# Kernel tuning notes

Hardware: AMD Instinct MI355X
Metric: run time of the kernel (lower is better)

## Reference

```python
import jax, jax.numpy as jnp
import numpy as np

N_NODES = 50000
N_EDGES = 800000
D_IN, D_HID, D_OUT = 128, 128, 64


def setup_inputs() -> dict:
    key = jax.random.key(0)
    ks = jax.random.split(key, 10)
    return {
        "x": jax.random.normal(ks[0], (N_NODES, D_IN), dtype=jnp.float32),
        "edge_row": jax.random.randint(ks[1], (N_EDGES,), 0, N_NODES, dtype=jnp.int32),
        "edge_col": jax.random.randint(ks[2], (N_EDGES,), 0, N_NODES, dtype=jnp.int32),
        "edge_val": jax.random.uniform(ks[3], (N_EDGES,), dtype=jnp.float32),
        "W1": jax.random.normal(ks[4], (D_IN, D_HID), dtype=jnp.float32) * (1.0 / np.sqrt(D_HID)),
        "b1": jax.random.normal(ks[5], (D_HID,), dtype=jnp.float32) * (1.0 / np.sqrt(D_HID)),
        "W2": jax.random.normal(ks[6], (D_HID, D_HID), dtype=jnp.float32) * (1.0 / np.sqrt(D_HID)),
        "b2": jax.random.normal(ks[7], (D_HID,), dtype=jnp.float32) * (1.0 / np.sqrt(D_HID)),
        "W3": jax.random.normal(ks[8], (D_HID, D_OUT), dtype=jnp.float32) * (1.0 / np.sqrt(D_OUT)),
        "b3": jax.random.normal(ks[9], (D_OUT,), dtype=jnp.float32) * (1.0 / np.sqrt(D_OUT)),
    }


def _gcn_layer(x, edge_row, edge_col, edge_val, W, b):
    # support = x @ W          : dense GEMM [N, d_out]
    support = x @ W
    # spmm(adj, support)[i] = sum_e with row[e]==i: val[e] * support[col[e]]
    gathered = support[edge_col] * edge_val[:, None]  # [E, d_out]
    agg = jax.ops.segment_sum(gathered, edge_row, num_segments=x.shape[0])
    return agg + b


def reference(x, edge_row, edge_col, edge_val, W1, b1, W2, b2, W3, b3):
    # Layer 1 + ReLU (dropout is identity in eval)
    h = jax.nn.relu(_gcn_layer(x, edge_row, edge_col, edge_val, W1, b1))
    # Layer 2 + ReLU
    h = jax.nn.relu(_gcn_layer(h, edge_row, edge_col, edge_val, W2, b2))
    # Layer 3 (no activation)
    return _gcn_layer(h, edge_row, edge_col, edge_val, W3, b3)
```

## Files before the change

### kernel.cpp

```cpp
#include <hip/hip_runtime.h>

#define N_NODES 50000
#define N_EDGES 800000
#define GEMM1_BLOCKS 704
#define FUSED_BLOCKS 512
#define FILL_BLOCKS ((N_EDGES + 255) / 256)
#define SCAN_BLOCKS ((N_NODES + 255) / 256)

#define HB 64
#define EPB (N_EDGES / HB)
#define HGROUPS (EPB / 4)
#define HWORDS (N_NODES / 4)

static_assert(N_NODES < 65536, "col must fit in 16 bits for packed CSR");
static_assert(N_EDGES % (4 * HB) == 0, "chunking must be exact");

typedef __attribute__((ext_vector_type(4))) float f32x4;
typedef __attribute__((ext_vector_type(8))) short bf16x8;

__device__ inline unsigned short f32_to_bf16(float f) {
    unsigned int u = __builtin_bit_cast(unsigned int, f);
    u += 0x7FFF + ((u >> 16) & 1);
    return (unsigned short)(u >> 16);
}
__device__ inline float bf16_to_f32(unsigned short h) {
    unsigned int u = ((unsigned int)h) << 16;
    return __builtin_bit_cast(float, u);
}

template <int NOUT>
__device__ __forceinline__ void mfma_phase(const unsigned short* Xs,
                                           const unsigned short* Ws,
                                           unsigned short* __restrict__ Yb,
                                           int block_row, int N) {
    constexpr int KP = 128 + 8;
    constexpr int NT = NOUT / 16;
    const int tid = threadIdx.x;
    const int wave = tid >> 6;
    const int lane = tid & 63;
    const int m = lane & 15;
    const int quad = lane >> 4;
    const int rowbase = wave * 16;

    f32x4 acc[NT];
#pragma unroll
    for (int t = 0; t < NT; ++t) acc[t] = (f32x4){0.f, 0.f, 0.f, 0.f};

#pragma unroll
    for (int kt = 0; kt < 4; ++kt) {
        bf16x8 a = *reinterpret_cast<const bf16x8*>(
            Xs + (rowbase + m) * KP + kt * 32 + quad * 8);
#pragma unroll
        for (int t = 0; t < NT; ++t) {
            bf16x8 b = *reinterpret_cast<const bf16x8*>(
                Ws + (t * 16 + m) * KP + kt * 32 + quad * 8);
            acc[t] = __builtin_amdgcn_mfma_f32_16x16x32_bf16(a, b, acc[t], 0, 0, 0);
        }
    }

#pragma unroll
    for (int t = 0; t < NT; ++t) {
#pragma unroll
        for (int r = 0; r < 4; ++r) {
            int grow = block_row + rowbase + quad * 4 + r;
            if (grow < N)
                Yb[(size_t)grow * NOUT + t * 16 + m] = f32_to_bf16(acc[t][r]);
        }
    }
}

__global__ __launch_bounds__(256) void mega1(
    const float* __restrict__ x, const float* __restrict__ W1,
    unsigned short* __restrict__ Yb, int N, int ntiles_g,
    const int* __restrict__ erow, unsigned int* __restrict__ rank8,
    unsigned int* __restrict__ bhist) {
    constexpr int KP = 128 + 8;
    __shared__ __align__(16) unsigned char smem[52224];
    const int tid = threadIdx.x;

    if (blockIdx.x < HB) {
        const int b = blockIdx.x;
        unsigned int* h = reinterpret_cast<unsigned int*>(smem);
        int4* h4 = reinterpret_cast<int4*>(h);
        for (int i = tid; i < HWORDS / 4; i += 256) {
            int4 z = {0, 0, 0, 0};
            h4[i] = z;
        }
        __syncthreads();
        const int4* eg = reinterpret_cast<const int4*>(erow) + (size_t)b * HGROUPS;
        unsigned int* rg = rank8 + (size_t)b * HGROUPS;
        for (int g = tid; g < HGROUPS; g += 256) {
            int4 er = eg[g];
            unsigned int rk;
            int sh;
            unsigned int o;
            sh = (er.x & 3) << 3;
            o = atomicAdd(&h[er.x >> 2], 1u << sh);
            rk = (o >> sh) & 0xFFu;
            sh = (er.y & 3) << 3;
            o = atomicAdd(&h[er.y >> 2], 1u << sh);
            rk |= ((o >> sh) & 0xFFu) << 8;
            sh = (er.z & 3) << 3;
            o = atomicAdd(&h[er.z >> 2], 1u << sh);
            rk |= ((o >> sh) & 0xFFu) << 16;
            sh = (er.w & 3) << 3;
            o = atomicAdd(&h[er.w >> 2], 1u << sh);
            rk |= ((o >> sh) & 0xFFu) << 24;
            rg[g] = rk;
        }
        __syncthreads();
        int4* dst = reinterpret_cast<int4*>(bhist + (size_t)b * HWORDS);
        for (int i = tid; i < HWORDS / 4; i += 256) dst[i] = h4[i];
        return;
    }

    const int gb = blockIdx.x - HB;
    unsigned short* Xs = reinterpret_cast<unsigned short*>(smem);
    unsigned short* Ws = reinterpret_cast<unsigned short*>(smem) + 64 * KP;

    for (int idx = tid; idx < 128 * 128; idx += 256) {
        int k = idx >> 7, m = idx & 127;
        Ws[m * KP + k] = f32_to_bf16(W1[idx]);
    }

    for (int tile = gb; tile < ntiles_g; tile += GEMM1_BLOCKS) {
        const int block_row = tile * 64;
        for (int idx = tid; idx < 64 * 16; idx += 256) {
            int r = idx >> 4, ch = idx & 15;
            int gr = block_row + r;
            if (gr >= N) gr = N - 1;
            const float4* xp =
                reinterpret_cast<const float4*>(x + (size_t)gr * 128 + ch * 8);
            float4 a = xp[0], b2 = xp[1];
            uint4 o;
            o.x = (unsigned int)f32_to_bf16(a.x) | ((unsigned int)f32_to_bf16(a.y) << 16);
            o.y = (unsigned int)f32_to_bf16(a.z) | ((unsigned int)f32_to_bf16(a.w) << 16);
            o.z = (unsigned int)f32_to_bf16(b2.x) | ((unsigned int)f32_to_bf16(b2.y) << 16);
            o.w = (unsigned int)f32_to_bf16(b2.z) | ((unsigned int)f32_to_bf16(b2.w) << 16);
            *reinterpret_cast<uint4*>(Xs + r * KP + ch * 8) = o;
        }
        __syncthreads();
        mfma_phase<128>(Xs, Ws, Yb, block_row, N);
        __syncthreads();
    }
}

__global__ void scan1(const unsigned int* __restrict__ bhist,
                      int* __restrict__ pref, int* __restrict__ btot, int n) {
    __shared__ int sums[256];
    const int t = threadIdx.x;
    const int b = blockIdx.x;
    const int node = b * 256 + t;
    const unsigned char* bh8 = reinterpret_cast<const unsigned char*>(bhist);
    int deg = 0;
    if (node < n) {
        for (int c = 0; c < HB; ++c) deg += bh8[(size_t)c * N_NODES + node];
    }
    sums[t] = deg;
    __syncthreads();
    for (int off = 1; off < 256; off <<= 1) {
        int x = (t >= off) ? sums[t - off] : 0;
        __syncthreads();
        sums[t] += x;
        __syncthreads();
    }
    if (node < n) pref[node] = sums[t] - deg;
    if (t == 255) btot[b] = sums[255];
}

__global__ void scan2(const unsigned int* __restrict__ bhist,
                      const int* __restrict__ pref, const int* __restrict__ btot,
                      int* __restrict__ rptr, int* __restrict__ bbase,
                      int n, int nblocks) {
    __shared__ int off_s, tot_s;
    const int t = threadIdx.x;
    const int b = blockIdx.x;
    const int node = b * 256 + t;
    if (t == 0) {
        int off = 0, tot = 0;
        for (int i = 0; i < nblocks; ++i) {
            int v = btot[i];
            if (i < b) off += v;
            tot += v;
        }
        off_s = off;
        tot_s = tot;
    }
    __syncthreads();
    if (node < n) {
        int run = off_s + pref[node];
        rptr[node] = run;
        const unsigned char* bh8 = reinterpret_cast<const unsigned char*>(bhist);
        for (int c = 0; c < HB; ++c) {
            bbase[(size_t)c * N_NODES + node] = run;
            run += bh8[(size_t)c * N_NODES + node];
        }
    }
    if (b == 0 && t == 0) rptr[n] = tot_s;
}

__global__ void fill_csr(const int* __restrict__ erow, const int* __restrict__ ecol,
                         const float* __restrict__ eval, const int* __restrict__ bbase,
                         const unsigned int* __restrict__ rank8,
                         unsigned int* __restrict__ cpack) {
    int e = blockIdx.x * blockDim.x + threadIdx.x;
    if (e >= N_EDGES) return;
    const unsigned char* r8 = reinterpret_cast<const unsigned char*>(rank8);
    int slot = bbase[(size_t)(e / EPB) * N_NODES + erow[e]] + r8[e];
    unsigned int p = (unsigned int)(ecol[e] & 0xFFFF) |
                     ((unsigned int)f32_to_bf16(eval[e]) << 16);
    cpack[slot] = p;
}

template <int NOUT>
__device__ __forceinline__ void mfma_phase512(const unsigned short* Xs,
                                              const unsigned short* Ws,
                                              unsigned short* __restrict__ Yb,
                                              int block_row, int N) {
    constexpr int KP = 128 + 8;
    constexpr int NT = NOUT / 16;
    constexpr int NTH = NT / 2;
    const int tid = threadIdx.x;
    const int wave = tid >> 6;
    const int lane = tid & 63;
    const int m = lane & 15;
    const int quad = lane >> 4;
    const int rowbase = (wave & 3) * 16;
    const int tbase = (wave >> 2) * NTH;

    f32x4 acc[NTH];
#pragma unroll
    for (int t = 0; t < NTH; ++t) acc[t] = (f32x4){0.f, 0.f, 0.f, 0.f};

#pragma unroll
    for (int kt = 0; kt < 4; ++kt) {
        bf16x8 a = *reinterpret_cast<const bf16x8*>(
            Xs + (rowbase + m) * KP + kt * 32 + quad * 8);
#pragma unroll
        for (int t = 0; t < NTH; ++t) {
            bf16x8 b = *reinterpret_cast<const bf16x8*>(
                Ws + ((tbase + t) * 16 + m) * KP + kt * 32 + quad * 8);
            acc[t] = __builtin_amdgcn_mfma_f32_16x16x32_bf16(a, b, acc[t], 0, 0, 0);
        }
    }

#pragma unroll
    for (int t = 0; t < NTH; ++t) {
#pragma unroll
        for (int r = 0; r < 4; ++r) {
            int grow = block_row + rowbase + quad * 4 + r;
            if (grow < N)
                Yb[(size_t)grow * NOUT + (tbase + t) * 16 + m] = f32_to_bf16(acc[t][r]);
        }
    }
}

template <int NOUT>
__global__ __launch_bounds__(512, 4) void gemm_fused_agg(
    const unsigned short* __restrict__ S,
    const int* __restrict__ rptr, const unsigned int* __restrict__ cpack,
    const float* __restrict__ bias,
    const float* __restrict__ W,
    unsigned short* __restrict__ Yb,
    int N, int ntiles) {
    constexpr int KP = 128 + 8;
    __shared__ unsigned short Xs[64 * KP];
    __shared__ unsigned short Ws[NOUT * KP];
    __shared__ unsigned int cp_s[2048];
    const int tid = threadIdx.x;
    const int group = tid >> 4;
    const int f8 = tid & 15;

    for (int idx = tid; idx < 128 * NOUT; idx += 512) {
        int k = idx / NOUT, m = idx % NOUT;
        Ws[m * KP + k] = f32_to_bf16(W[idx]);
    }

    float bv[8];
#pragma unroll
    for (int i = 0; i < 8; ++i) bv[i] = bias[f8 * 8 + i];

    for (int tile = blockIdx.x; tile < ntiles; tile += gridDim.x) {
        const int block_row = tile * 64;
        const int rend = (block_row + 64 < N) ? block_row + 64 : N;
        const int ebeg = rptr[block_row];
        const int ecount = rptr[rend] - ebeg;
        __syncthreads();
        for (int i = tid; i < ecount; i += 512) cp_s[i] = cpack[ebeg + i];
        __syncthreads();
#pragma unroll
        for (int r4 = 0; r4 < 2; ++r4) {
            const int row = r4 * 32 + group;
            const int node = block_row + row;
            float acc[8];
#pragma unroll
            for (int i = 0; i < 8; ++i) acc[i] = bv[i];
            if (node < N) {
                const int beg = rptr[node] - ebeg;
                const int end = rptr[node + 1] - ebeg;
                int j = beg;
                for (; j + 8 <= end; j += 8) {
                    unsigned int p[8];
                    uint4 s[8];
#pragma unroll
                    for (int u = 0; u < 8; ++u) p[u] = cp_s[j + u];
#pragma unroll
                    for (int u = 0; u < 8; ++u)
                        s[u] = *reinterpret_cast<const uint4*>(
                            S + (size_t)(p[u] & 0xFFFF) * 128 + f8 * 8);
#pragma unroll
                    for (int u = 0; u < 8; ++u) {
                        const float v = bf16_to_f32((unsigned short)(p[u] >> 16));
                        const unsigned short* sp =
                            reinterpret_cast<const unsigned short*>(&s[u]);
#pragma unroll
                        for (int i = 0; i < 8; ++i)
                            acc[i] = fmaf(v, bf16_to_f32(sp[i]), acc[i]);
                    }
                }
                if (j + 4 <= end) {
                    unsigned int p[4];
                    uint4 s[4];
#pragma unroll
                    for (int u = 0; u < 4; ++u) p[u] = cp_s[j + u];
#pragma unroll
                    for (int u = 0; u < 4; ++u)
                        s[u] = *reinterpret_cast<const uint4*>(
                            S + (size_t)(p[u] & 0xFFFF) * 128 + f8 * 8);
#pragma unroll
                    for (int u = 0; u < 4; ++u) {
                        const float v = bf16_to_f32((unsigned short)(p[u] >> 16));
                        const unsigned short* sp =
                            reinterpret_cast<const unsigned short*>(&s[u]);
#pragma unroll
                        for (int i = 0; i < 8; ++i)
                            acc[i] = fmaf(v, bf16_to_f32(sp[i]), acc[i]);
                    }
                    j += 4;
                }
                if (j + 2 <= end) {
                    unsigned int p[2];
                    uint4 s[2];
#pragma unroll
                    for (int u = 0; u < 2; ++u) p[u] = cp_s[j + u];
#pragma unroll
                    for (int u = 0; u < 2; ++u)
                        s[u] = *reinterpret_cast<const uint4*>(
                            S + (size_t)(p[u] & 0xFFFF) * 128 + f8 * 8);
#pragma unroll
                    for (int u = 0; u < 2; ++u) {
                        const float v = bf16_to_f32((unsigned short)(p[u] >> 16));
                        const unsigned short* sp =
                            reinterpret_cast<const unsigned short*>(&s[u]);
#pragma unroll
                        for (int i = 0; i < 8; ++i)
                            acc[i] = fmaf(v, bf16_to_f32(sp[i]), acc[i]);
                    }
                    j += 2;
                }
                if (j < end) {
                    unsigned int p = cp_s[j];
                    uint4 s = *reinterpret_cast<const uint4*>(
                        S + (size_t)(p & 0xFFFF) * 128 + f8 * 8);
                    const float v = bf16_to_f32((unsigned short)(p >> 16));
                    const unsigned short* sp =
                        reinterpret_cast<const unsigned short*>(&s);
#pragma unroll
                    for (int i = 0; i < 8; ++i)
                        acc[i] = fmaf(v, bf16_to_f32(sp[i]), acc[i]);
                }
            }
            uint4 o;
            o.x = (unsigned int)f32_to_bf16(fmaxf(acc[0], 0.f)) |
                  ((unsigned int)f32_to_bf16(fmaxf(acc[1], 0.f)) << 16);
            o.y = (unsigned int)f32_to_bf16(fmaxf(acc[2], 0.f)) |
                  ((unsigned int)f32_to_bf16(fmaxf(acc[3], 0.f)) << 16);
            o.z = (unsigned int)f32_to_bf16(fmaxf(acc[4], 0.f)) |
                  ((unsigned int)f32_to_bf16(fmaxf(acc[5], 0.f)) << 16);
            o.w = (unsigned int)f32_to_bf16(fmaxf(acc[6], 0.f)) |
                  ((unsigned int)f32_to_bf16(fmaxf(acc[7], 0.f)) << 16);
            *reinterpret_cast<uint4*>(Xs + row * KP + f8 * 8) = o;
        }
        __syncthreads();
        mfma_phase512<NOUT>(Xs, Ws, Yb, block_row, N);
    }
}

__global__ void aggregate_bf16_64(const unsigned short* __restrict__ S,
                                  const int* __restrict__ rptr,
                                  const unsigned int* __restrict__ cpack,
                                  const float* __restrict__ bias,
                                  float* __restrict__ out, int N) {
    __shared__ unsigned int cp_s[1536];
    const int t = threadIdx.x;
    const int nfirst = blockIdx.x * 32;
    const int node = nfirst + (t >> 3);
    const int f8 = t & 7;
    const int nlast1 = (nfirst + 32 < N) ? nfirst + 32 : N;
    int ebeg = 0, ecount = 0;
    if (nfirst < N) {
        ebeg = rptr[nfirst];
        ecount = rptr[nlast1] - ebeg;
    }
    for (int i = t; i < ecount; i += 256) cp_s[i] = cpack[ebeg + i];
    __syncthreads();
    if (node >= N) return;
    int j = rptr[node] - ebeg;
    const int end = rptr[node + 1] - ebeg;
    float acc[8];
#pragma unroll
    for (int i = 0; i < 8; ++i) acc[i] = bias[f8 * 8 + i];
    for (; j + 8 <= end; j += 8) {
        unsigned int p[8];
        uint4 s[8];
#pragma unroll
        for (int u = 0; u < 8; ++u) p[u] = cp_s[j + u];
#pragma unroll
        for (int u = 0; u < 8; ++u)
            s[u] = *reinterpret_cast<const uint4*>(S + (size_t)(p[u] & 0xFFFF) * 64 + f8 * 8);
#pragma unroll
        for (int u = 0; u < 8; ++u) {
            const float v = bf16_to_f32((unsigned short)(p[u] >> 16));
            const unsigned short* sp = reinterpret_cast<const unsigned short*>(&s[u]);
#pragma unroll
            for (int i = 0; i < 8; ++i) acc[i] = fmaf(v, bf16_to_f32(sp[i]), acc[i]);
        }
    }
    if (j + 4 <= end) {
        unsigned int p[4];
        uint4 s[4];
#pragma unroll
        for (int u = 0; u < 4; ++u) p[u] = cp_s[j + u];
#pragma unroll
        for (int u = 0; u < 4; ++u)
            s[u] = *reinterpret_cast<const uint4*>(S + (size_t)(p[u] & 0xFFFF) * 64 + f8 * 8);
#pragma unroll
        for (int u = 0; u < 4; ++u) {
            const float v = bf16_to_f32((unsigned short)(p[u] >> 16));
            const unsigned short* sp = reinterpret_cast<const unsigned short*>(&s[u]);
#pragma unroll
            for (int i = 0; i < 8; ++i) acc[i] = fmaf(v, bf16_to_f32(sp[i]), acc[i]);
        }
        j += 4;
    }
    if (j + 2 <= end) {
        unsigned int p[2];
        uint4 s[2];
#pragma unroll
        for (int u = 0; u < 2; ++u) p[u] = cp_s[j + u];
#pragma unroll
        for (int u = 0; u < 2; ++u)
            s[u] = *reinterpret_cast<const uint4*>(S + (size_t)(p[u] & 0xFFFF) * 64 + f8 * 8);
#pragma unroll
        for (int u = 0; u < 2; ++u) {
            const float v = bf16_to_f32((unsigned short)(p[u] >> 16));
            const unsigned short* sp = reinterpret_cast<const unsigned short*>(&s[u]);
#pragma unroll
            for (int i = 0; i < 8; ++i) acc[i] = fmaf(v, bf16_to_f32(sp[i]), acc[i]);
        }
        j += 2;
    }
    if (j < end) {
        unsigned int p = cp_s[j];
        uint4 s = *reinterpret_cast<const uint4*>(S + (size_t)(p & 0xFFFF) * 64 + f8 * 8);
        const float v = bf16_to_f32((unsigned short)(p >> 16));
        const unsigned short* sp = reinterpret_cast<const unsigned short*>(&s);
#pragma unroll
        for (int i = 0; i < 8; ++i) acc[i] = fmaf(v, bf16_to_f32(sp[i]), acc[i]);
    }
    float4 o0 = {acc[0], acc[1], acc[2], acc[3]};
    float4 o1 = {acc[4], acc[5], acc[6], acc[7]};
    float* op = out + (size_t)node * 64 + f8 * 8;
    *reinterpret_cast<float4*>(op) = o0;
    *reinterpret_cast<float4*>(op + 4) = o1;
}

extern "C" void kernel_launch(void* const* d_in, const int* in_sizes, int n_in,
                              void* d_out, int out_size, void* d_ws, size_t ws_size,
                              hipStream_t stream) {
    const float* x    = (const float*)d_in[0];
    const int*   erow = (const int*)d_in[1];
    const int*   ecol = (const int*)d_in[2];
    const float* eval = (const float*)d_in[3];
    const float* W1   = (const float*)d_in[4];
    const float* b1   = (const float*)d_in[5];
    const float* W2   = (const float*)d_in[6];
    const float* b2   = (const float*)d_in[7];
    const float* W3   = (const float*)d_in[8];
    const float* b3   = (const float*)d_in[9];
    float* out = (float*)d_out;

    const size_t nf = (size_t)N_NODES * 128;
    unsigned short* SA   = (unsigned short*)d_ws;
    unsigned short* SB   = SA + nf;
    unsigned int*  rank8 = (unsigned int*)(SB + nf);
    unsigned int*  bhist = rank8 + N_EDGES / 4;
    int*   bbase  = (int*)(bhist + (size_t)HB * HWORDS);
    int*   rptr   = bbase + (size_t)HB * N_NODES;
    unsigned int* cpack = (unsigned int*)(rptr + N_NODES + 1);
    int*   pref   = (int*)(cpack + N_EDGES);
    int*   btot   = pref + N_NODES;

    const int blk = 256;
    const int ntiles_g = (N_NODES + 63) / 64;
    const int agg_grid = (int)(((long long)N_NODES * 8 + blk - 1) / blk);

    mega1<<<HB + GEMM1_BLOCKS, blk, 0, stream>>>(
        x, W1, SA, N_NODES, ntiles_g, erow, rank8, bhist);

    scan1<<<SCAN_BLOCKS, blk, 0, stream>>>(bhist, pref, btot, N_NODES);
    scan2<<<SCAN_BLOCKS, blk, 0, stream>>>(bhist, pref, btot, rptr, bbase,
                                           N_NODES, SCAN_BLOCKS);

    fill_csr<<<FILL_BLOCKS, blk, 0, stream>>>(erow, ecol, eval, bbase, rank8, cpack);

    gemm_fused_agg<128><<<FUSED_BLOCKS, 512, 0, stream>>>(
        SA, rptr, cpack, b1, W2, SB, N_NODES, ntiles_g);

    gemm_fused_agg<64><<<FUSED_BLOCKS, 512, 0, stream>>>(
        SB, rptr, cpack, b2, W3, SA, N_NODES, ntiles_g);

    aggregate_bf16_64<<<agg_grid, blk, 0, stream>>>(SA, rptr, cpack, b3, out, N_NODES);
}
```

Measured before the change: 218.8 us.

## Fuse CSR scan and fill into mega1 with grid-wide atomic barriers

Merges the two scan kernels and the CSR fill kernel into the first GEMM/histogram kernel. Histogram blocks use device-scope atomic counters as spin barriers to do the degree scan cooperatively, and then all blocks wait before filling the packed CSR. The per-chunk base offsets are now stored as 8-bit cumulative counts (cum8) instead of 32-bit bbase, and the fill processes four edges per thread with vector loads. This removes three kernel launches and shrinks workspace traffic. In exchange it relies on all 768 blocks being co-resident to avoid deadlock, and the GEMM blocks must idle until the scan finishes.

```diff
diff --git a/kernel.cpp b/kernel.cpp
--- a/kernel.cpp
+++ b/kernel.cpp
@@ -4,13 +4,15 @@
 #define N_EDGES 800000
 #define GEMM1_BLOCKS 704
 #define FUSED_BLOCKS 512
-#define FILL_BLOCKS ((N_EDGES + 255) / 256)
-#define SCAN_BLOCKS ((N_NODES + 255) / 256)
 
 #define HB 64
 #define EPB (N_EDGES / HB)
 #define HGROUPS (EPB / 4)
 #define HWORDS (N_NODES / 4)
+#define NGROUPS (N_EDGES / 4)
+#define TOTB (HB + GEMM1_BLOCKS)
+#define GPB ((NGROUPS + TOTB - 1) / TOTB)
+#define SCAN_NPB 800
 
 static_assert(N_NODES < 65536, "col must fit in 16 bits for packed CSR");
 static_assert(N_EDGES % (4 * HB) == 0, "chunking must be exact");
@@ -72,14 +74,20 @@
 __global__ __launch_bounds__(256) void mega1(
     const float* __restrict__ x, const float* __restrict__ W1,
     unsigned short* __restrict__ Yb, int N, int ntiles_g,
-    const int* __restrict__ erow, unsigned int* __restrict__ rank8,
-    unsigned int* __restrict__ bhist) {
+    const int* __restrict__ erow, const int* __restrict__ ecol,
+    const float* __restrict__ eval,
+    unsigned int* __restrict__ rank8, unsigned int* __restrict__ bhist,
+    unsigned char* __restrict__ cum8, int* __restrict__ rptr,
+    unsigned int* __restrict__ cpack, int* __restrict__ btot,
+    int* __restrict__ c_hist, int* __restrict__ c_s1, int* __restrict__ c_s2) {
     constexpr int KP = 128 + 8;
     __shared__ __align__(16) unsigned char smem[52224];
+    __shared__ int off_s;
     const int tid = threadIdx.x;
-
-    if (blockIdx.x < HB) {
-        const int b = blockIdx.x;
+    const int b = blockIdx.x;
+
+    if (b < HB) {
+        if (b == 0 && tid == 0) { *c_hist = 0; *c_s1 = 0; *c_s2 = 0; }
         unsigned int* h = reinterpret_cast<unsigned int*>(smem);
         int4* h4 = reinterpret_cast<int4*>(h);
         for (int i = tid; i < HWORDS / 4; i += 256) {
@@ -111,105 +119,141 @@
         __syncthreads();
         int4* dst = reinterpret_cast<int4*>(bhist + (size_t)b * HWORDS);
         for (int i = tid; i < HWORDS / 4; i += 256) dst[i] = h4[i];
-        return;
-    }
-
-    const int gb = blockIdx.x - HB;
-    unsigned short* Xs = reinterpret_cast<unsigned short*>(smem);
-    unsigned short* Ws = reinterpret_cast<unsigned short*>(smem) + 64 * KP;
-
-    for (int idx = tid; idx < 128 * 128; idx += 256) {
-        int k = idx >> 7, m = idx & 127;
-        Ws[m * KP + k] = f32_to_bf16(W1[idx]);
-    }
-
-    for (int tile = gb; tile < ntiles_g; tile += GEMM1_BLOCKS) {
-        const int block_row = tile * 64;
-        for (int idx = tid; idx < 64 * 16; idx += 256) {
-            int r = idx >> 4, ch = idx & 15;
-            int gr = block_row + r;
-            if (gr >= N) gr = N - 1;
-            const float4* xp =
-                reinterpret_cast<const float4*>(x + (size_t)gr * 128 + ch * 8);
-            float4 a = xp[0], b2 = xp[1];
-            uint4 o;
-            o.x = (unsigned int)f32_to_bf16(a.x) | ((unsigned int)f32_to_bf16(a.y) << 16);
-            o.y = (unsigned int)f32_to_bf16(a.z) | ((unsigned int)f32_to_bf16(a.w) << 16);
-            o.z = (unsigned int)f32_to_bf16(b2.x) | ((unsigned int)f32_to_bf16(b2.y) << 16);
-            o.w = (unsigned int)f32_to_bf16(b2.z) | ((unsigned int)f32_to_bf16(b2.w) << 16);
-            *reinterpret_cast<uint4*>(Xs + r * KP + ch * 8) = o;
-        }
-        __syncthreads();
-        mfma_phase<128>(Xs, Ws, Yb, block_row, N);
-        __syncthreads();
-    }
-}
-
-__global__ void scan1(const unsigned int* __restrict__ bhist,
-                      int* __restrict__ pref, int* __restrict__ btot, int n) {
-    __shared__ int sums[256];
-    const int t = threadIdx.x;
-    const int b = blockIdx.x;
-    const int node = b * 256 + t;
-    const unsigned char* bh8 = reinterpret_cast<const unsigned char*>(bhist);
-    int deg = 0;
-    if (node < n) {
-        for (int c = 0; c < HB; ++c) deg += bh8[(size_t)c * N_NODES + node];
-    }
-    sums[t] = deg;
+        __threadfence();
+        if (tid == 0) atomicAdd(c_hist, 1);
+
+        int* deg_s = reinterpret_cast<int*>(smem);
+        int* sums = deg_s + SCAN_NPB;
+        const int nbase = b * SCAN_NPB;
+        int nlen = N - nbase;
+        if (nlen > SCAN_NPB) nlen = SCAN_NPB;
+        if (nlen < 0) nlen = 0;
+        if (tid == 0) {
+            while (__hip_atomic_load(c_hist, __ATOMIC_ACQUIRE,
+                                     __HIP_MEMORY_SCOPE_AGENT) < HB)
+                __builtin_amdgcn_s_sleep(8);
+        }
+        __syncthreads();
+        __threadfence();
+        const unsigned char* bh8 = reinterpret_cast<const unsigned char*>(bhist);
+        for (int i = tid; i < nlen; i += 256) {
+            int node = nbase + i;
+            int d = 0;
+            for (int c = 0; c < HB; ++c) d += bh8[(size_t)c * N_NODES + node];
+            deg_s[i] = d;
+        }
+        __syncthreads();
+        const int base4 = tid * 4;
+        int v[4], my = 0;
+#pragma unroll
+        for (int k = 0; k < 4; ++k) {
+            v[k] = (base4 + k < nlen) ? deg_s[base4 + k] : 0;
+            my += v[k];
+        }
+        sums[tid] = my;
+        __syncthreads();
+        for (int off = 1; off < 256; off <<= 1) {
+            int xx = (tid >= off) ? sums[tid - off] : 0;
+            __syncthreads();
+            sums[tid] += xx;
+            __syncthreads();
+        }
+        int run = sums[tid] - my;
+        const int blktot = sums[255];
+#pragma unroll
+        for (int k = 0; k < 4; ++k) {
+            if (base4 + k < nlen) deg_s[base4 + k] = run;
+            run += v[k];
+        }
+        __syncthreads();
+        if (tid == 0) {
+            btot[b] = blktot;
+            __threadfence();
+            atomicAdd(c_s1, 1);
+            while (__hip_atomic_load(c_s1, __ATOMIC_ACQUIRE,
+                                     __HIP_MEMORY_SCOPE_AGENT) < HB)
+                __builtin_amdgcn_s_sleep(8);
+            __threadfence();
+            int off = 0, tot = 0;
+            for (int i = 0; i < HB; ++i) {
+                int t2 = btot[i];
+                if (i < b) off += t2;
+                tot += t2;
+            }
+            off_s = off;
+            if (b == 0) rptr[N] = tot;
+        }
+        __syncthreads();
+        for (int i = tid; i < nlen; i += 256) {
+            int node = nbase + i;
+            int rp = off_s + deg_s[i];
+            rptr[node] = rp;
+            unsigned int cum = 0;
+            for (int c = 0; c < HB; ++c) {
+                cum8[(size_t)c * N_NODES + node] = (unsigned char)cum;
+                cum += bh8[(size_t)c * N_NODES + node];
+            }
+        }
+        __threadfence();
+        __syncthreads();
+        if (tid == 0) atomicAdd(c_s2, 1);
+    } else {
+        const int gb = b - HB;
+        unsigned short* Xs = reinterpret_cast<unsigned short*>(smem);
+        unsigned short* Ws = reinterpret_cast<unsigned short*>(smem) + 64 * KP;
+
+        for (int idx = tid; idx < 128 * 128; idx += 256) {
+            int k = idx >> 7, m = idx & 127;
+            Ws[m * KP + k] = f32_to_bf16(W1[idx]);
+        }
+
+        for (int tile = gb; tile < ntiles_g; tile += GEMM1_BLOCKS) {
+            const int block_row = tile * 64;
+            for (int idx = tid; idx < 64 * 16; idx += 256) {
+                int r = idx >> 4, ch = idx & 15;
+                int gr = block_row + r;
+                if (gr >= N) gr = N - 1;
+                const float4* xp =
+                    reinterpret_cast<const float4*>(x + (size_t)gr * 128 + ch * 8);
+                float4 a = xp[0], b2 = xp[1];
+                uint4 o;
+                o.x = (unsigned int)f32_to_bf16(a.x) | ((unsigned int)f32_to_bf16(a.y) << 16);
+                o.y = (unsigned int)f32_to_bf16(a.z) | ((unsigned int)f32_to_bf16(a.w) << 16);
+                o.z = (unsigned int)f32_to_bf16(b2.x) | ((unsigned int)f32_to_bf16(b2.y) << 16);
+                o.w = (unsigned int)f32_to_bf16(b2.z) | ((unsigned int)f32_to_bf16(b2.w) << 16);
+                *reinterpret_cast<uint4*>(Xs + r * KP + ch * 8) = o;
+            }
+            __syncthreads();
+            mfma_phase<128>(Xs, Ws, Yb, block_row, N);
+            __syncthreads();
+        }
+    }
+
+    if (tid == 0) {
+        while (__hip_atomic_load(c_s2, __ATOMIC_ACQUIRE,
+                                 __HIP_MEMORY_SCOPE_AGENT) < HB)
+            __builtin_amdgcn_s_sleep(8);
+    }
     __syncthreads();
-    for (int off = 1; off < 256; off <<= 1) {
-        int x = (t >= off) ? sums[t - off] : 0;
-        __syncthreads();
-        sums[t] += x;
-        __syncthreads();
-    }
-    if (node < n) pref[node] = sums[t] - deg;
-    if (t == 255) btot[b] = sums[255];
-}
-
-__global__ void scan2(const unsigned int* __restrict__ bhist,
-                      const int* __restrict__ pref, const int* __restrict__ btot,
-                      int* __restrict__ rptr, int* __restrict__ bbase,
-                      int n, int nblocks) {
-    __shared__ int off_s, tot_s;
-    const int t = threadIdx.x;
-    const int b = blockIdx.x;
-    const int node = b * 256 + t;
-    if (t == 0) {
-        int off = 0, tot = 0;
-        for (int i = 0; i < nblocks; ++i) {
-            int v = btot[i];
-            if (i < b) off += v;
-            tot += v;
-        }
-        off_s = off;
-        tot_s = tot;
-    }
-    __syncthreads();
-    if (node < n) {
-        int run = off_s + pref[node];
-        rptr[node] = run;
-        const unsigned char* bh8 = reinterpret_cast<const unsigned char*>(bhist);
-        for (int c = 0; c < HB; ++c) {
-            bbase[(size_t)c * N_NODES + node] = run;
-            run += bh8[(size_t)c * N_NODES + node];
-        }
-    }
-    if (b == 0 && t == 0) rptr[n] = tot_s;
-}
-
-__global__ void fill_csr(const int* __restrict__ erow, const int* __restrict__ ecol,
-                         const float* __restrict__ eval, const int* __restrict__ bbase,
-                         const unsigned int* __restrict__ rank8,
-                         unsigned int* __restrict__ cpack) {
-    int e = blockIdx.x * blockDim.x + threadIdx.x;
-    if (e >= N_EDGES) return;
-    const unsigned char* r8 = reinterpret_cast<const unsigned char*>(rank8);
-    int slot = bbase[(size_t)(e / EPB) * N_NODES + erow[e]] + r8[e];
-    unsigned int p = (unsigned int)(ecol[e] & 0xFFFF) |
-                     ((unsigned int)f32_to_bf16(eval[e]) << 16);
-    cpack[slot] = p;
+    __threadfence();
+    int gbeg = b * GPB;
+    int gend = gbeg + GPB;
+    if (gend > NGROUPS) gend = NGROUPS;
+    for (int g = gbeg + tid; g < gend; g += 256) {
+        int4 er = reinterpret_cast<const int4*>(erow)[g];
+        int4 ec = reinterpret_cast<const int4*>(ecol)[g];
+        float4 ev = reinterpret_cast<const float4*>(eval)[g];
+        unsigned int rk = rank8[g];
+        const unsigned char* cb = cum8 + (size_t)(g / HGROUPS) * N_NODES;
+        int s0 = rptr[er.x] + cb[er.x] + (int)(rk & 0xFF);
+        int s1 = rptr[er.y] + cb[er.y] + (int)((rk >> 8) & 0xFF);
+        int s2 = rptr[er.z] + cb[er.z] + (int)((rk >> 16) & 0xFF);
+        int s3 = rptr[er.w] + cb[er.w] + (int)(rk >> 24);
+        cpack[s0] = (unsigned int)(ec.x & 0xFFFF) | ((unsigned int)f32_to_bf16(ev.x) << 16);
+        cpack[s1] = (unsigned int)(ec.y & 0xFFFF) | ((unsigned int)f32_to_bf16(ev.y) << 16);
+        cpack[s2] = (unsigned int)(ec.z & 0xFFFF) | ((unsigned int)f32_to_bf16(ev.z) << 16);
+        cpack[s3] = (unsigned int)(ec.w & 0xFFFF) | ((unsigned int)f32_to_bf16(ev.w) << 16);
+    }
 }
 
 template <int NOUT>
@@ -491,28 +535,25 @@
     float* out = (float*)d_out;
 
     const size_t nf = (size_t)N_NODES * 128;
-    unsigned short* SA   = (unsigned short*)d_ws;
-    unsigned short* SB   = SA + nf;
-    unsigned int*  rank8 = (unsigned int*)(SB + nf);
-    unsigned int*  bhist = rank8 + N_EDGES / 4;
-    int*   bbase  = (int*)(bhist + (size_t)HB * HWORDS);
-    int*   rptr   = bbase + (size_t)HB * N_NODES;
+    unsigned short* SA    = (unsigned short*)d_ws;
+    unsigned short* SB    = SA + nf;
+    unsigned int*   rank8 = (unsigned int*)(SB + nf);
+    unsigned int*   bhist = rank8 + NGROUPS;
+    unsigned char*  cum8  = (unsigned char*)(bhist + (size_t)HB * HWORDS);
+    int*   rptr   = (int*)(cum8 + (size_t)HB * N_NODES);
     unsigned int* cpack = (unsigned int*)(rptr + N_NODES + 1);
-    int*   pref   = (int*)(cpack + N_EDGES);
-    int*   btot   = pref + N_NODES;
+    int*   btot   = (int*)(cpack + N_EDGES);
+    int*   c_hist = btot + HB + 16;
+    int*   c_s1   = btot + HB + 32;
+    int*   c_s2   = btot + HB + 48;
 
     const int blk = 256;
     const int ntiles_g = (N_NODES + 63) / 64;
     const int agg_grid = (int)(((long long)N_NODES * 8 + blk - 1) / blk);
 
-    mega1<<<HB + GEMM1_BLOCKS, blk, 0, stream>>>(
-        x, W1, SA, N_NODES, ntiles_g, erow, rank8, bhist);
-
-    scan1<<<SCAN_BLOCKS, blk, 0, stream>>>(bhist, pref, btot, N_NODES);
-    scan2<<<SCAN_BLOCKS, blk, 0, stream>>>(bhist, pref, btot, rptr, bbase,
-                                           N_NODES, SCAN_BLOCKS);
-
-    fill_csr<<<FILL_BLOCKS, blk, 0, stream>>>(erow, ecol, eval, bbase, rank8, cpack);
+    mega1<<<TOTB, blk, 0, stream>>>(
+        x, W1, SA, N_NODES, ntiles_g, erow, ecol, eval, rank8, bhist,
+        cum8, rptr, cpack, btot, c_hist, c_s1, c_s2);
 
     gemm_fused_agg<128><<<FUSED_BLOCKS, 512, 0, stream>>>(
         SA, rptr, cpack, b1, W2, SB, N_NODES, ntiles_g);
```

Result: slower. 560.4 us (+156.1%).
